# Kernel optimization log

Measured on AMD Instinct MI355X. Metric: run time of the kernel, lower is better.

Reference implementation:

```python
import jax, jax.numpy as jnp
import numpy as np

N = 50000      # nodes
E = 800000     # directed edges (avg degree 16)
IN, HID, OUT = 128, 128, 64


def setup_inputs() -> dict:
    key = jax.random.key(0)
    k1, k2, k3, k4 = jax.random.split(key, 4)
    x = jax.random.normal(k1, (N, IN), dtype=jnp.float32)
    edge_index = jax.random.randint(k2, (2, E), 0, N, dtype=jnp.int64)
    W1 = jax.random.normal(k3, (IN, HID), dtype=jnp.float32) * (1.0 / np.sqrt(IN))
    b1 = jnp.zeros((HID,), dtype=jnp.float32)
    W2 = jax.random.normal(k4, (HID, OUT), dtype=jnp.float32) * (1.0 / np.sqrt(HID))
    b2 = jnp.zeros((OUT,), dtype=jnp.float32)
    return {"x": x, "edge_index": edge_index, "W1": W1, "b1": b1, "W2": W2, "b2": b2}


def _gcn_conv(x, src, dst, norm, W, b, n):
    # linear transform first (PyG GCNConv), then normalized scatter-add aggregation
    h = x @ W                                  # [N, d_out]
    msg = h[src] * norm[:, None]               # [E', d_out] gathered edge messages
    return jax.ops.segment_sum(msg, dst, num_segments=n) + b


def reference(x, edge_index, W1, b1, W2, b2):
    n = x.shape[0]
    loops = jnp.arange(n, dtype=edge_index.dtype)
    src = jnp.concatenate([edge_index[0], loops])  # source (row)
    dst = jnp.concatenate([edge_index[1], loops])  # target (col)
    # symmetric normalization on A + I: deg over destination nodes
    deg = jax.ops.segment_sum(jnp.ones_like(src, dtype=x.dtype), dst, num_segments=n)
    dinv = jnp.where(deg > 0, jax.lax.rsqrt(deg), 0.0)
    norm = dinv[src] * dinv[dst]               # [E']
    h = jax.nn.relu(_gcn_conv(x, src, dst, norm, W1, b1, n))
    out = _gcn_conv(h, src, dst, norm, W2, b2, n)
    return jax.nn.log_softmax(out, axis=1)
```

## Files before the change

kernel.cpp:

```cpp
#include <hip/hip_runtime.h>


constexpr int K1 = 128;
constexpr int CAP = 64;

typedef short short8 __attribute__((ext_vector_type(8)));
typedef float f32x4 __attribute__((ext_vector_type(4)));

__device__ inline unsigned short f2b(float f) {
    unsigned u = __float_as_uint(f);
    u += 0x7fffu + ((u >> 16) & 1u);
    return (unsigned short)(u >> 16);
}

__global__ void k_init(int* __restrict__ cur, const float* __restrict__ W1,
                       const float* __restrict__ W2, unsigned short* __restrict__ w1bt,
                       unsigned short* __restrict__ w2bt, int n) {
    int i = blockIdx.x * blockDim.x + threadIdx.x;
    if (i < n) cur[i] = 0;
    if (i < 128 * 128) {
        int c = i >> 7, k = i & 127;
        w1bt[i] = f2b(W1[k * 128 + c]);
    }
    if (i < 64 * 128) {
        int c = i >> 7, k = i & 127;
        w2bt[i] = f2b(W2[k * 64 + c]);
    }
}

__device__ __forceinline__ void gemm128_body(int bid, const float* __restrict__ A,
                                             const unsigned short* __restrict__ Wbt,
                                             unsigned short* __restrict__ Cb, int n) {
    constexpr int NT = 8;
    const int tid = threadIdx.x;
    const int wave = tid >> 6, lane = tid & 63;
    const int rowbase = bid * 128 + wave * 32;
    const int lrow = lane & 15;
    const int kgrp = lane >> 4;

    short8 a[2][4];
#pragma unroll
    for (int s = 0; s < 2; ++s)
#pragma unroll
        for (int kt = 0; kt < 4; ++kt) {
            int R = rowbase + 16 * s + lrow;
            int Rc = (R < n) ? R : (n - 1);
            const float* p = A + (size_t)Rc * 128 + kt * 32 + kgrp * 8;
            float4 u0 = *reinterpret_cast<const float4*>(p);
            float4 u1 = *reinterpret_cast<const float4*>(p + 4);
            short8 af;
            af[0] = (short)f2b(u0.x); af[1] = (short)f2b(u0.y);
            af[2] = (short)f2b(u0.z); af[3] = (short)f2b(u0.w);
            af[4] = (short)f2b(u1.x); af[5] = (short)f2b(u1.y);
            af[6] = (short)f2b(u1.z); af[7] = (short)f2b(u1.w);
            a[s][kt] = af;
        }

    f32x4 acc[2][NT];
#pragma unroll
    for (int s = 0; s < 2; ++s)
#pragma unroll
        for (int nt = 0; nt < NT; ++nt) acc[s][nt] = f32x4{0.f, 0.f, 0.f, 0.f};

#pragma unroll
    for (int nt = 0; nt < NT; ++nt) {
        short8 b[4];
#pragma unroll
        for (int kt = 0; kt < 4; ++kt)
            b[kt] = *reinterpret_cast<const short8*>(
                Wbt + (size_t)(nt * 16 + lrow) * 128 + kt * 32 + kgrp * 8);
#pragma unroll
        for (int s = 0; s < 2; ++s)
#pragma unroll
            for (int kt = 0; kt < 4; ++kt)
                acc[s][nt] = __builtin_amdgcn_mfma_f32_16x16x32_bf16(a[s][kt], b[kt],
                                                                     acc[s][nt], 0, 0, 0);
    }

#pragma unroll
    for (int s = 0; s < 2; ++s)
#pragma unroll
        for (int r = 0; r < 4; ++r) {
            int R = rowbase + 16 * s + kgrp * 4 + r;
            if (R < n) {
#pragma unroll
                for (int nt = 0; nt < NT; ++nt)
                    Cb[(size_t)R * 128 + nt * 16 + lrow] = f2b(acc[s][nt][r]);
            }
        }
}

__global__ __launch_bounds__(256) void k_gemm_fill(
    const float* __restrict__ A, const unsigned short* __restrict__ Wbt,
    unsigned short* __restrict__ Cb, int n,
    const int* __restrict__ src, const int* __restrict__ dst,
    int* __restrict__ cur, unsigned short* __restrict__ csr, int e, int ngemm) {
    int b = blockIdx.x;
    if (b < ngemm) {
        gemm128_body(b, A, Wbt, Cb, n);
    } else {
        int i = (b - ngemm) * blockDim.x + threadIdx.x;
        if (i < e) {
            int d = dst[i];
            int p = atomicAdd(&cur[d], 1);
            if (p < CAP) csr[(size_t)d * CAP + p] = (unsigned short)src[i];
        }
    }
}

__global__ __launch_bounds__(256) void k_gemm64(
    const unsigned short* __restrict__ Ab, const unsigned short* __restrict__ Wbt,
    const int* __restrict__ cur, unsigned short* __restrict__ Cb, int n) {
    constexpr int NT = 4;
    const int tid = threadIdx.x;
    const int wave = tid >> 6, lane = tid & 63;
    const int rowbase = blockIdx.x * 128 + wave * 32;
    const int lrow = lane & 15;
    const int kgrp = lane >> 4;

    short8 a[2][4];
#pragma unroll
    for (int s = 0; s < 2; ++s)
#pragma unroll
        for (int kt = 0; kt < 4; ++kt) {
            int R = rowbase + 16 * s + lrow;
            int Rc = (R < n) ? R : (n - 1);
            a[s][kt] = *reinterpret_cast<const short8*>(
                Ab + (size_t)Rc * 128 + kt * 32 + kgrp * 8);
        }

    f32x4 acc[2][NT];
#pragma unroll
    for (int s = 0; s < 2; ++s)
#pragma unroll
        for (int nt = 0; nt < NT; ++nt) acc[s][nt] = f32x4{0.f, 0.f, 0.f, 0.f};

#pragma unroll
    for (int nt = 0; nt < NT; ++nt) {
        short8 b[4];
#pragma unroll
        for (int kt = 0; kt < 4; ++kt)
            b[kt] = *reinterpret_cast<const short8*>(
                Wbt + (size_t)(nt * 16 + lrow) * 128 + kt * 32 + kgrp * 8);
#pragma unroll
        for (int s = 0; s < 2; ++s)
#pragma unroll
            for (int kt = 0; kt < 4; ++kt)
                acc[s][nt] = __builtin_amdgcn_mfma_f32_16x16x32_bf16(a[s][kt], b[kt],
                                                                     acc[s][nt], 0, 0, 0);
    }

#pragma unroll
    for (int s = 0; s < 2; ++s)
#pragma unroll
        for (int r = 0; r < 4; ++r) {
            int R = rowbase + 16 * s + kgrp * 4 + r;
            if (R < n) {
                float sc = rsqrtf((float)(cur[R] + 1));
#pragma unroll
                for (int nt = 0; nt < NT; ++nt)
                    Cb[(size_t)R * 64 + nt * 16 + lrow] = f2b(sc * acc[s][nt][r]);
            }
        }
}

__global__ __launch_bounds__(256) void k_gather128(
    const int* __restrict__ cur, const unsigned short* __restrict__ csr,
    const unsigned short* __restrict__ xb, const float* __restrict__ b,
    unsigned short* __restrict__ agg, int n) {
    int wid = (blockIdx.x * blockDim.x + threadIdx.x) >> 6;
    int lane = threadIdx.x & 63;
    if (wid >= n) return;
    const int q = lane >> 4;
    const int c0 = (lane & 15) * 8;

    float a[8];
#pragma unroll
    for (int k = 0; k < 8; ++k) a[k] = 0.f;

    const size_t s0 = (size_t)wid * CAP;
    int cnt = cur[wid];
    if (cnt > CAP) cnt = CAP;

    int t = q;
    for (; t + 4 < cnt; t += 8) {
        int e0 = csr[s0 + t];
        int e1 = csr[s0 + t + 4];
        float d0 = rsqrtf((float)(cur[e0] + 1));
        float d1 = rsqrtf((float)(cur[e1] + 1));
        uint4 v0 = *reinterpret_cast<const uint4*>(xb + (size_t)e0 * 128 + c0);
        uint4 v1 = *reinterpret_cast<const uint4*>(xb + (size_t)e1 * 128 + c0);
#pragma unroll
        for (int j = 0; j < 4; ++j) {
            unsigned w0 = (&v0.x)[j];
            unsigned w1 = (&v1.x)[j];
            a[2 * j]     = fmaf(d0, __uint_as_float(w0 << 16), a[2 * j]);
            a[2 * j + 1] = fmaf(d0, __uint_as_float(w0 & 0xffff0000u), a[2 * j + 1]);
            a[2 * j]     = fmaf(d1, __uint_as_float(w1 << 16), a[2 * j]);
            a[2 * j + 1] = fmaf(d1, __uint_as_float(w1 & 0xffff0000u), a[2 * j + 1]);
        }
    }
    for (; t < cnt; t += 4) {
        int e0 = csr[s0 + t];
        float d0 = rsqrtf((float)(cur[e0] + 1));
        uint4 v0 = *reinterpret_cast<const uint4*>(xb + (size_t)e0 * 128 + c0);
#pragma unroll
        for (int j = 0; j < 4; ++j) {
            unsigned w0 = (&v0.x)[j];
            a[2 * j]     = fmaf(d0, __uint_as_float(w0 << 16), a[2 * j]);
            a[2 * j + 1] = fmaf(d0, __uint_as_float(w0 & 0xffff0000u), a[2 * j + 1]);
        }
    }

#pragma unroll
    for (int k = 0; k < 8; ++k) {
        a[k] += __shfl_xor(a[k], 16);
        a[k] += __shfl_xor(a[k], 32);
    }

    if (q == 0) {
        float di = rsqrtf((float)(cnt + 1));
        uint4 sv = *reinterpret_cast<const uint4*>(xb + (size_t)wid * 128 + c0);
        float4 bv0 = *reinterpret_cast<const float4*>(b + c0);
        float4 bv1 = *reinterpret_cast<const float4*>(b + c0 + 4);
        float o[8];
#pragma unroll
        for (int j = 0; j < 4; ++j) {
            unsigned w = (&sv.x)[j];
            o[2 * j]     = fmaf(di, __uint_as_float(w << 16), a[2 * j]);
            o[2 * j + 1] = fmaf(di, __uint_as_float(w & 0xffff0000u), a[2 * j + 1]);
        }
        const float* bb0 = (const float*)&bv0;
        const float* bb1 = (const float*)&bv1;
        short8 st;
#pragma unroll
        for (int k = 0; k < 8; ++k) {
            float bk = (k < 4) ? bb0[k] : bb1[k - 4];
            st[k] = (short)f2b(fmaxf(fmaf(di, o[k], bk), 0.f));
        }
        *reinterpret_cast<short8*>(agg + (size_t)wid * 128 + c0) = st;
    }
}

__global__ __launch_bounds__(256) void k_gather64_lsm(
    const int* __restrict__ cur, const unsigned short* __restrict__ csr,
    const unsigned short* __restrict__ hb, const float* __restrict__ b,
    float* __restrict__ out, int n) {
    int wid = (blockIdx.x * blockDim.x + threadIdx.x) >> 6;
    int lane = threadIdx.x & 63;
    if (wid >= n) return;
    const int oct = lane >> 3;
    const int c0 = (lane & 7) * 8;

    float a[8];
#pragma unroll
    for (int k = 0; k < 8; ++k) a[k] = 0.f;

    const size_t s0 = (size_t)wid * CAP;
    int cnt = cur[wid];
    if (cnt > CAP) cnt = CAP;

    int t = oct;
    for (; t + 8 < cnt; t += 16) {
        int e0 = csr[s0 + t];
        int e1 = csr[s0 + t + 8];
        uint4 v0 = *reinterpret_cast<const uint4*>(hb + (size_t)e0 * 64 + c0);
        uint4 v1 = *reinterpret_cast<const uint4*>(hb + (size_t)e1 * 64 + c0);
#pragma unroll
        for (int j = 0; j < 4; ++j) {
            unsigned w0 = (&v0.x)[j];
            unsigned w1 = (&v1.x)[j];
            a[2 * j]     += __uint_as_float(w0 << 16);
            a[2 * j + 1] += __uint_as_float(w0 & 0xffff0000u);
            a[2 * j]     += __uint_as_float(w1 << 16);
            a[2 * j + 1] += __uint_as_float(w1 & 0xffff0000u);
        }
    }
    for (; t < cnt; t += 8) {
        int e0 = csr[s0 + t];
        uint4 v0 = *reinterpret_cast<const uint4*>(hb + (size_t)e0 * 64 + c0);
#pragma unroll
        for (int j = 0; j < 4; ++j) {
            unsigned w0 = (&v0.x)[j];
            a[2 * j]     += __uint_as_float(w0 << 16);
            a[2 * j + 1] += __uint_as_float(w0 & 0xffff0000u);
        }
    }

#pragma unroll
    for (int k = 0; k < 8; ++k) {
        a[k] += __shfl_xor(a[k], 8);
        a[k] += __shfl_xor(a[k], 16);
        a[k] += __shfl_xor(a[k], 32);
    }

    float di = rsqrtf((float)(cnt + 1));
    uint4 sv = *reinterpret_cast<const uint4*>(hb + (size_t)wid * 64 + c0);
    float4 bv0 = *reinterpret_cast<const float4*>(b + c0);
    float4 bv1 = *reinterpret_cast<const float4*>(b + c0 + 4);
    float v[8];
#pragma unroll
    for (int j = 0; j < 4; ++j) {
        unsigned w = (&sv.x)[j];
        v[2 * j]     = a[2 * j]     + __uint_as_float(w << 16);
        v[2 * j + 1] = a[2 * j + 1] + __uint_as_float(w & 0xffff0000u);
    }
    v[0] = fmaf(di, v[0], bv0.x);
    v[1] = fmaf(di, v[1], bv0.y);
    v[2] = fmaf(di, v[2], bv0.z);
    v[3] = fmaf(di, v[3], bv0.w);
    v[4] = fmaf(di, v[4], bv1.x);
    v[5] = fmaf(di, v[5], bv1.y);
    v[6] = fmaf(di, v[6], bv1.z);
    v[7] = fmaf(di, v[7], bv1.w);

    float m = v[0];
#pragma unroll
    for (int k = 1; k < 8; ++k) m = fmaxf(m, v[k]);
    m = fmaxf(m, __shfl_xor(m, 1));
    m = fmaxf(m, __shfl_xor(m, 2));
    m = fmaxf(m, __shfl_xor(m, 4));

    float s = 0.f;
#pragma unroll
    for (int k = 0; k < 8; ++k) s += expf(v[k] - m);
    s += __shfl_xor(s, 1);
    s += __shfl_xor(s, 2);
    s += __shfl_xor(s, 4);
    float ls = m + logf(s);

    if (oct == 0) {
        float4 r0, r1;
        r0.x = v[0] - ls; r0.y = v[1] - ls; r0.z = v[2] - ls; r0.w = v[3] - ls;
        r1.x = v[4] - ls; r1.y = v[5] - ls; r1.z = v[6] - ls; r1.w = v[7] - ls;
        *reinterpret_cast<float4*>(out + (size_t)wid * 64 + c0) = r0;
        *reinterpret_cast<float4*>(out + (size_t)wid * 64 + c0 + 4) = r1;
    }
}

extern "C" void kernel_launch(void* const* d_in, const int* in_sizes, int n_in,
                              void* d_out, int out_size, void* d_ws, size_t ws_size,
                              hipStream_t stream) {
    const float* x  = (const float*)d_in[0];
    const int*   ei = (const int*)d_in[1];
    const float* W1 = (const float*)d_in[2];
    const float* b1 = (const float*)d_in[3];
    const float* W2 = (const float*)d_in[4];
    const float* b2 = (const float*)d_in[5];

    const int n = in_sizes[0] / K1;
    const int e = in_sizes[1] / 2;
    const int* src = ei;
    const int* dst = ei + e;
    float* out = (float*)d_out;

    const int ngemm = (n + 127) / 128;
    const int nfill = (e + 255) / 256;

    unsigned short* agg1 = (unsigned short*)d_ws;
    unsigned short* xb16 = agg1 + (size_t)n * 128;
    unsigned short* hb16 = xb16 + (size_t)n * 128;
    int*            cur  = (int*)(hb16 + (size_t)n * 64);
    unsigned short* w1bt = (unsigned short*)(cur + n);
    unsigned short* w2bt = w1bt + 128 * 128;
    unsigned short* csr  = w2bt + 64 * 128;

    const int B = 256;

    k_init<<<(n + B - 1) / B, B, 0, stream>>>(cur, W1, W2, w1bt, w2bt, n);
    k_gemm_fill<<<ngemm + nfill, B, 0, stream>>>(x, w1bt, xb16, n,
                                                 src, dst, cur, csr, e, ngemm);
    k_gather128<<<(n + 3) / 4, B, 0, stream>>>(cur, csr, xb16, b1, agg1, n);
    k_gemm64<<<ngemm, B, 0, stream>>>(agg1, w2bt, cur, hb16, n);
    k_gather64_lsm<<<(n + 3) / 4, B, 0, stream>>>(cur, csr, hb16, b2, out, n);
}
```

Before: 124.3 us.

## Fuse second-layer GEMM into first-layer gather via per-wave LDS row

Removes the separate MFMA GEMM kernel for layer 2 and computes the 128x64 transform inside the layer-1 gather kernel. Each wave writes its ReLU'd aggregated row to LDS in fp32, then each lane computes one output column with scalar FMAs against bf16 W2. This drops the agg1 intermediate write/read and one launch, and keeps the row in fp32 instead of rounding it to bf16. In exchange, the matmul runs on scalar FMAs instead of MFMA, and every wave reads a full 16KB W2 (mostly from cache).

```diff
diff --git a/kernel.cpp b/kernel.cpp
--- a/kernel.cpp
+++ b/kernel.cpp
@@ -108,68 +108,15 @@
     }
 }
 
-__global__ __launch_bounds__(256) void k_gemm64(
-    const unsigned short* __restrict__ Ab, const unsigned short* __restrict__ Wbt,
-    const int* __restrict__ cur, unsigned short* __restrict__ Cb, int n) {
-    constexpr int NT = 4;
-    const int tid = threadIdx.x;
-    const int wave = tid >> 6, lane = tid & 63;
-    const int rowbase = blockIdx.x * 128 + wave * 32;
-    const int lrow = lane & 15;
-    const int kgrp = lane >> 4;
-
-    short8 a[2][4];
-#pragma unroll
-    for (int s = 0; s < 2; ++s)
-#pragma unroll
-        for (int kt = 0; kt < 4; ++kt) {
-            int R = rowbase + 16 * s + lrow;
-            int Rc = (R < n) ? R : (n - 1);
-            a[s][kt] = *reinterpret_cast<const short8*>(
-                Ab + (size_t)Rc * 128 + kt * 32 + kgrp * 8);
-        }
-
-    f32x4 acc[2][NT];
-#pragma unroll
-    for (int s = 0; s < 2; ++s)
-#pragma unroll
-        for (int nt = 0; nt < NT; ++nt) acc[s][nt] = f32x4{0.f, 0.f, 0.f, 0.f};
-
-#pragma unroll
-    for (int nt = 0; nt < NT; ++nt) {
-        short8 b[4];
-#pragma unroll
-        for (int kt = 0; kt < 4; ++kt)
-            b[kt] = *reinterpret_cast<const short8*>(
-                Wbt + (size_t)(nt * 16 + lrow) * 128 + kt * 32 + kgrp * 8);
-#pragma unroll
-        for (int s = 0; s < 2; ++s)
-#pragma unroll
-            for (int kt = 0; kt < 4; ++kt)
-                acc[s][nt] = __builtin_amdgcn_mfma_f32_16x16x32_bf16(a[s][kt], b[kt],
-                                                                     acc[s][nt], 0, 0, 0);
-    }
-
-#pragma unroll
-    for (int s = 0; s < 2; ++s)
-#pragma unroll
-        for (int r = 0; r < 4; ++r) {
-            int R = rowbase + 16 * s + kgrp * 4 + r;
-            if (R < n) {
-                float sc = rsqrtf((float)(cur[R] + 1));
-#pragma unroll
-                for (int nt = 0; nt < NT; ++nt)
-                    Cb[(size_t)R * 64 + nt * 16 + lrow] = f2b(sc * acc[s][nt][r]);
-            }
-        }
-}
-
-__global__ __launch_bounds__(256) void k_gather128(
+__global__ __launch_bounds__(256) void k_gather128_g64(
     const int* __restrict__ cur, const unsigned short* __restrict__ csr,
-    const unsigned short* __restrict__ xb, const float* __restrict__ b,
-    unsigned short* __restrict__ agg, int n) {
+    const unsigned short* __restrict__ xb, const float* __restrict__ b1,
+    const unsigned short* __restrict__ w2bt, unsigned short* __restrict__ hb, int n) {
+    __shared__ float rowlds[4][128];
+
     int wid = (blockIdx.x * blockDim.x + threadIdx.x) >> 6;
     int lane = threadIdx.x & 63;
+    int wave = threadIdx.x >> 6;
     if (wid >= n) return;
     const int q = lane >> 4;
     const int c0 = (lane & 15) * 8;
@@ -218,11 +165,14 @@
         a[k] += __shfl_xor(a[k], 32);
     }
 
+    const float di = rsqrtf((float)(cnt + 1));
+
     if (q == 0) {
-        float di = rsqrtf((float)(cnt + 1));
         uint4 sv = *reinterpret_cast<const uint4*>(xb + (size_t)wid * 128 + c0);
-        float4 bv0 = *reinterpret_cast<const float4*>(b + c0);
-        float4 bv1 = *reinterpret_cast<const float4*>(b + c0 + 4);
+        float4 bv0 = *reinterpret_cast<const float4*>(b1 + c0);
+        float4 bv1 = *reinterpret_cast<const float4*>(b1 + c0 + 4);
+        const float* bb0 = (const float*)&bv0;
+        const float* bb1 = (const float*)&bv1;
         float o[8];
 #pragma unroll
         for (int j = 0; j < 4; ++j) {
@@ -230,16 +180,34 @@
             o[2 * j]     = fmaf(di, __uint_as_float(w << 16), a[2 * j]);
             o[2 * j + 1] = fmaf(di, __uint_as_float(w & 0xffff0000u), a[2 * j + 1]);
         }
-        const float* bb0 = (const float*)&bv0;
-        const float* bb1 = (const float*)&bv1;
-        short8 st;
 #pragma unroll
         for (int k = 0; k < 8; ++k) {
             float bk = (k < 4) ? bb0[k] : bb1[k - 4];
-            st[k] = (short)f2b(fmaxf(fmaf(di, o[k], bk), 0.f));
-        }
-        *reinterpret_cast<short8*>(agg + (size_t)wid * 128 + c0) = st;
-    }
+            rowlds[wave][c0 + k] = fmaxf(fmaf(di, o[k], bk), 0.f);
+        }
+    }
+    __builtin_amdgcn_wave_barrier();
+    asm volatile("s_waitcnt lgkmcnt(0)" ::: "memory");
+    __builtin_amdgcn_sched_barrier(0);
+
+    float acc = 0.f;
+    const unsigned short* wc = w2bt + (size_t)lane * 128;
+    const float* row = rowlds[wave];
+#pragma unroll
+    for (int kk = 0; kk < 16; ++kk) {
+        float4 r0 = *reinterpret_cast<const float4*>(&row[kk * 8]);
+        float4 r1 = *reinterpret_cast<const float4*>(&row[kk * 8 + 4]);
+        uint4 wv = *reinterpret_cast<const uint4*>(wc + kk * 8);
+        acc = fmaf(r0.x, __uint_as_float(wv.x << 16), acc);
+        acc = fmaf(r0.y, __uint_as_float(wv.x & 0xffff0000u), acc);
+        acc = fmaf(r0.z, __uint_as_float(wv.y << 16), acc);
+        acc = fmaf(r0.w, __uint_as_float(wv.y & 0xffff0000u), acc);
+        acc = fmaf(r1.x, __uint_as_float(wv.z << 16), acc);
+        acc = fmaf(r1.y, __uint_as_float(wv.z & 0xffff0000u), acc);
+        acc = fmaf(r1.z, __uint_as_float(wv.w << 16), acc);
+        acc = fmaf(r1.w, __uint_as_float(wv.w & 0xffff0000u), acc);
+    }
+    hb[(size_t)wid * 64 + lane] = f2b(di * acc);
 }
 
 __global__ __launch_bounds__(256) void k_gather64_lsm(
@@ -357,8 +325,7 @@
     const int ngemm = (n + 127) / 128;
     const int nfill = (e + 255) / 256;
 
-    unsigned short* agg1 = (unsigned short*)d_ws;
-    unsigned short* xb16 = agg1 + (size_t)n * 128;
+    unsigned short* xb16 = (unsigned short*)d_ws;
     unsigned short* hb16 = xb16 + (size_t)n * 128;
     int*            cur  = (int*)(hb16 + (size_t)n * 64);
     unsigned short* w1bt = (unsigned short*)(cur + n);
@@ -370,7 +337,6 @@
     k_init<<<(n + B - 1) / B, B, 0, stream>>>(cur, W1, W2, w1bt, w2bt, n);
     k_gemm_fill<<<ngemm + nfill, B, 0, stream>>>(x, w1bt, xb16, n,
                                                  src, dst, cur, csr, e, ngemm);
-    k_gather128<<<(n + 3) / 4, B, 0, stream>>>(cur, csr, xb16, b1, agg1, n);
-    k_gemm64<<<ngemm, B, 0, stream>>>(agg1, w2bt, cur, hb16, n);
+    k_gather128_g64<<<(n + 3) / 4, B, 0, stream>>>(cur, csr, xb16, b1, w2bt, hb16, n);
     k_gather64_lsm<<<(n + 3) / 4, B, 0, stream>>>(cur, csr, hb16, b2, out, n);
 }
```

After: 193.3 us. +55.5%, slower.
